# Kernel optimization log

Measured on AMD Instinct MI355X. Metric: run time of the kernel, lower is better.

Reference implementation:

```python
import jax, jax.numpy as jnp
import numpy as np

B, L, D, H, HD = 2, 2048, 768, 12, 64
NEG = -1e9

def _rotate_half(x):
    x1, x2 = jnp.split(x, 2, axis=-1)
    return jnp.concatenate([-x2, x1], axis=-1)

def setup_inputs() -> dict:
    key = jax.random.key(0)
    ks = jax.random.split(key, 8)
    hidden_states = jax.random.normal(ks[0], (B, L, D), dtype=jnp.float32)
    # additive causal mask [B,1,L,L]
    causal = jnp.where(jnp.tril(jnp.ones((L, L), dtype=bool)), 0.0, NEG).astype(jnp.float32)
    attention_mask = jnp.broadcast_to(causal[None, None], (B, 1, L, L))
    # RoPE tables [B, L, HD]
    inv_freq = 1.0 / (10000.0 ** (jnp.arange(0, HD, 2, dtype=jnp.float32) / HD))
    angles = jnp.arange(L, dtype=jnp.float32)[:, None] * inv_freq[None, :]  # [L, HD/2]
    emb = jnp.concatenate([angles, angles], axis=-1)  # [L, HD]
    cos = jnp.broadcast_to(jnp.cos(emb)[None], (B, L, HD))
    sin = jnp.broadcast_to(jnp.sin(emb)[None], (B, L, HD))
    s = 0.02
    Wq = s * jax.random.normal(ks[1], (H * HD, D), dtype=jnp.float32)
    Wk = s * jax.random.normal(ks[2], (H * HD, D), dtype=jnp.float32)
    Wv = s * jax.random.normal(ks[3], (H * HD, D), dtype=jnp.float32)
    Wo = s * jax.random.normal(ks[4], (D, H * HD), dtype=jnp.float32)
    return {"hidden_states": hidden_states, "attention_mask": attention_mask,
            "cos": cos, "sin": sin, "Wq": Wq, "Wk": Wk, "Wv": Wv, "Wo": Wo}

def reference(hidden_states, attention_mask, cos, sin, Wq, Wk, Wv, Wo):
    b, l, _ = hidden_states.shape
    def proj(W):  # silu(x @ W.T) -> [B, H, L, HD]
        y = jax.nn.silu(jnp.einsum('bld,ed->ble', hidden_states, W))
        return y.reshape(b, l, H, HD).transpose(0, 2, 1, 3)
    q, k, v = proj(Wq), proj(Wk), proj(Wv)
    c = cos[:, None]  # [B,1,L,HD]
    s = sin[:, None]
    q = q * c + _rotate_half(q) * s
    k = k * c + _rotate_half(k) * s
    attn = jnp.einsum('bhqd,bhkd->bhqk', q, k)
    attn = attn + attention_mask
    attn = jax.nn.silu(attn) / l
    out = jnp.einsum('bhqk,bhkd->bhqd', attn, v)  # [B,H,L,HD]
    out = out.transpose(0, 2, 1, 3).reshape(b, l, H * HD)
    attn_output = jnp.einsum('ble,de->bld', out, Wo)
    return attn_output, attn
```

## Files before the change

kernel.cpp:

```cpp
#include <hip/hip_runtime.h>
#include <cstddef>

#define Bc   2
#define Lc   2048
#define Dc   768
#define Hc   12
#define HDc  64
#define Mrows (Bc * Lc)
#define PAD  72

typedef _Float16 half8 __attribute__((ext_vector_type(8)));
typedef unsigned short ushort8 __attribute__((ext_vector_type(8)));
typedef __attribute__((ext_vector_type(4))) float floatx4;

__device__ __forceinline__ float silu_f(float x) {
    return x / (1.0f + __expf(-x));
}
__device__ __forceinline__ unsigned short f2h(float x) {
    _Float16 h = (_Float16)x;
    return __builtin_bit_cast(unsigned short, h);
}
__device__ __forceinline__ float h2f(unsigned short u) {
    return (float)__builtin_bit_cast(_Float16, u);
}

template<int MODE>
__global__ __launch_bounds__(256)
void gemm_f16(const float* __restrict__ A32, const unsigned short* __restrict__ A16,
              const float* __restrict__ W, void* __restrict__ Cout) {
    __shared__ unsigned short Af[64][PAD];
    __shared__ unsigned short Wf[64][PAD];
    const int tid  = threadIdx.x;
    const int lane = tid & 63, w = tid >> 6;
    const int m    = lane & 15, quad = lane >> 4;
    const int m0 = blockIdx.y * 64, n0 = blockIdx.x * 64;

    floatx4 acc[4] = {{0.f,0.f,0.f,0.f},{0.f,0.f,0.f,0.f},
                      {0.f,0.f,0.f,0.f},{0.f,0.f,0.f,0.f}};

    for (int kc = 0; kc < Dc; kc += 64) {
        __syncthreads();
        if (MODE == 2) {
#pragma unroll
            for (int p = 0; p < 2; ++p) {
                const int f = tid + p * 256;
                const int row = f >> 3, c8 = (f & 7) << 3;
                const ushort8 t = *(const ushort8*)(A16 + (size_t)(m0 + row) * Dc + kc + c8);
                *(ushort8*)&Af[row][c8] = t;
            }
        } else {
#pragma unroll
            for (int p = 0; p < 4; ++p) {
                const int f = tid + p * 256;
                const int row = f >> 4, c4 = (f & 15) << 2;
                const float4 t = *(const float4*)(A32 + (size_t)(m0 + row) * Dc + kc + c4);
                const ushort4 hh = make_ushort4(f2h(t.x), f2h(t.y), f2h(t.z), f2h(t.w));
                *(ushort4*)&Af[row][c4] = hh;
            }
        }
#pragma unroll
        for (int p = 0; p < 4; ++p) {
            const int f = tid + p * 256;
            const int row = f >> 4, c4 = (f & 15) << 2;
            const float4 t = *(const float4*)(W + (size_t)(n0 + row) * Dc + kc + c4);
            const ushort4 hh = make_ushort4(f2h(t.x), f2h(t.y), f2h(t.z), f2h(t.w));
            *(ushort4*)&Wf[row][c4] = hh;
        }
        __syncthreads();

        const half8 a0 = *(const half8*)&Af[w * 16 + m][0 * 32 + quad * 8];
        const half8 a1 = *(const half8*)&Af[w * 16 + m][1 * 32 + quad * 8];
#pragma unroll
        for (int nn = 0; nn < 4; ++nn) {
            const half8 b0 = *(const half8*)&Wf[nn * 16 + m][0 * 32 + quad * 8];
            const half8 b1 = *(const half8*)&Wf[nn * 16 + m][1 * 32 + quad * 8];
            acc[nn] = __builtin_amdgcn_mfma_f32_16x16x32_f16(a0, b0, acc[nn], 0, 0, 0);
            acc[nn] = __builtin_amdgcn_mfma_f32_16x16x32_f16(a1, b1, acc[nn], 0, 0, 0);
        }
    }

#pragma unroll
    for (int nn = 0; nn < 4; ++nn) {
        const int col = n0 + nn * 16 + m;
        if (MODE == 0) {
            const int h = col >> 6, hd = col & 63;
            unsigned short* q16 = (unsigned short*)Cout;
#pragma unroll
            for (int r = 0; r < 4; ++r) {
                const int row = m0 + w * 16 + quad * 4 + r;
                const int b = row >> 11, l = row & (Lc - 1);
                q16[(((size_t)(b * Hc + h) * Lc + l) * HDc) + hd] = f2h(silu_f(acc[nn][r]));
            }
        } else if (MODE == 1) {
            const int h = col >> 6, hd = col & 63;
            unsigned short* vT16 = (unsigned short*)Cout;
            const int row0 = m0 + w * 16 + quad * 4;
            const int b = row0 >> 11, l0 = row0 & (Lc - 1);
            const ushort4 hh = make_ushort4(f2h(silu_f(acc[nn][0])), f2h(silu_f(acc[nn][1])),
                                            f2h(silu_f(acc[nn][2])), f2h(silu_f(acc[nn][3])));
            *(ushort4*)(vT16 + ((size_t)(b * Hc + h) * HDc + hd) * Lc + l0) = hh;
        } else {
            float* C = (float*)Cout;
#pragma unroll
            for (int r = 0; r < 4; ++r) {
                const int row = m0 + w * 16 + quad * 4 + r;
                C[(size_t)row * Dc + col] = acc[nn][r];
            }
        }
    }
}

__global__ __launch_bounds__(256)
void rope_kernel(unsigned short* __restrict__ q, unsigned short* __restrict__ k,
                 const float* __restrict__ cosb, const float* __restrict__ sinb) {
    const int idx = blockIdx.x * blockDim.x + threadIdx.x;
    const int total = Bc * Hc * Lc * 32;
    if (idx >= total) return;
    const int hd = idx & 31;
    const int l  = (idx >> 5) & (Lc - 1);
    const int h  = (idx >> 16) % Hc;
    const int b  = idx / (32 * Lc * Hc);
    unsigned short* arr = (blockIdx.y == 0) ? q : k;
    const size_t base  = (((size_t)b * Hc + h) * Lc + l) * HDc;
    const size_t cbase = ((size_t)b * Lc + l) * HDc;
    const float x1 = h2f(arr[base + hd]);
    const float x2 = h2f(arr[base + hd + 32]);
    const float c1 = cosb[cbase + hd],      s1 = sinb[cbase + hd];
    const float c2 = cosb[cbase + hd + 32], s2 = sinb[cbase + hd + 32];
    arr[base + hd]      = f2h(x1 * c1 - x2 * s1);
    arr[base + hd + 32] = f2h(x2 * c2 + x1 * s2);
}

__global__ __launch_bounds__(256)
void attn_kernel(const unsigned short* __restrict__ q16,
                 const unsigned short* __restrict__ k16,
                 const unsigned short* __restrict__ vT16,
                 float* __restrict__ attn_out,
                 unsigned short* __restrict__ o16) {
    __shared__ unsigned short Qf[64][PAD];
    __shared__ unsigned short Kf[64][PAD];
    __shared__ unsigned short Vt[64][PAD];
    __shared__ unsigned short Ps[64][PAD];

    const int tid  = threadIdx.x;
    const int lane = tid & 63, w = tid >> 6;
    const int m = lane & 15, quad = lane >> 4;
    const int qt = gridDim.x - 1 - blockIdx.x;
    const int bh = blockIdx.y;
    const int b = bh / Hc, h = bh % Hc;
    const size_t qkv = (size_t)bh * Lc * HDc;
    const float invL = 1.0f / (float)Lc;

    {
        const unsigned short* qp = q16 + qkv + (size_t)(qt * 64) * HDc;
#pragma unroll
        for (int p = 0; p < 2; ++p) {
            const int f = tid + p * 256;
            const int row = f >> 3, c8 = (f & 7) << 3;
            *(ushort8*)&Qf[row][c8] = *(const ushort8*)(qp + row * HDc + c8);
        }
    }
    __syncthreads();

    const half8 bq0 = *(const half8*)&Qf[w * 16 + m][0 * 32 + quad * 8];
    const half8 bq1 = *(const half8*)&Qf[w * 16 + m][1 * 32 + quad * 8];

    floatx4 oacc[4] = {{0.f,0.f,0.f,0.f},{0.f,0.f,0.f,0.f},
                       {0.f,0.f,0.f,0.f},{0.f,0.f,0.f,0.f}};
    float* attn_base = attn_out + (size_t)bh * Lc * Lc;

    for (int kt = 0; kt <= qt; ++kt) {
        __syncthreads();
        {
            const unsigned short* kp = k16 + qkv + (size_t)(kt * 64) * HDc;
            const unsigned short* vp = vT16 + (size_t)bh * HDc * Lc + kt * 64;
#pragma unroll
            for (int p = 0; p < 2; ++p) {
                const int f = tid + p * 256;
                const int row = f >> 3, c8 = (f & 7) << 3;
                *(ushort8*)&Kf[row][c8] = *(const ushort8*)(kp + row * HDc + c8);
                *(ushort8*)&Vt[row][c8] = *(const ushort8*)(vp + (size_t)row * Lc + c8);
            }
        }
        __syncthreads();

        const bool diag = (kt == qt);
        const int gi = qt * 64 + w * 16 + m;
#pragma unroll
        for (int mm = 0; mm < 4; ++mm) {
            const half8 ak0 = *(const half8*)&Kf[mm * 16 + m][0 * 32 + quad * 8];
            const half8 ak1 = *(const half8*)&Kf[mm * 16 + m][1 * 32 + quad * 8];
            floatx4 s = {0.f, 0.f, 0.f, 0.f};
            s = __builtin_amdgcn_mfma_f32_16x16x32_f16(ak0, bq0, s, 0, 0, 0);
            s = __builtin_amdgcn_mfma_f32_16x16x32_f16(ak1, bq1, s, 0, 0, 0);
            const int kj0 = mm * 16 + quad * 4;
            const int gj0 = kt * 64 + kj0;
            float v[4];
#pragma unroll
            for (int r = 0; r < 4; ++r) {
                float val = s[r];
                v[r] = (diag && (gj0 + r) > gi) ? 0.0f : silu_f(val) * invL;
            }
            *(float4*)(attn_base + (size_t)gi * Lc + gj0) = make_float4(v[0], v[1], v[2], v[3]);
            *(ushort4*)&Ps[w * 16 + m][kj0] = make_ushort4(f2h(v[0]), f2h(v[1]), f2h(v[2]), f2h(v[3]));
        }
        __syncthreads();

        const half8 ap0 = *(const half8*)&Ps[w * 16 + m][0 * 32 + quad * 8];
        const half8 ap1 = *(const half8*)&Ps[w * 16 + m][1 * 32 + quad * 8];
#pragma unroll
        for (int nn = 0; nn < 4; ++nn) {
            const half8 bv0 = *(const half8*)&Vt[nn * 16 + m][0 * 32 + quad * 8];
            const half8 bv1 = *(const half8*)&Vt[nn * 16 + m][1 * 32 + quad * 8];
            oacc[nn] = __builtin_amdgcn_mfma_f32_16x16x32_f16(ap0, bv0, oacc[nn], 0, 0, 0);
            oacc[nn] = __builtin_amdgcn_mfma_f32_16x16x32_f16(ap1, bv1, oacc[nn], 0, 0, 0);
        }
    }

    {
        const int tx = tid & 15, ty = tid >> 4;
#pragma unroll 1
        for (int kt2 = qt + 1; kt2 < Lc / 64; ++kt2) {
            const float4 z = make_float4(0.f, 0.f, 0.f, 0.f);
#pragma unroll
            for (int i = 0; i < 4; ++i) {
                const int gi2 = qt * 64 + (ty << 2) + i;
                *(float4*)(attn_base + (size_t)gi2 * Lc + kt2 * 64 + (tx << 2)) = z;
            }
        }
    }

#pragma unroll
    for (int nn = 0; nn < 4; ++nn)
#pragma unroll
        for (int r = 0; r < 4; ++r) {
            const int gi2 = qt * 64 + w * 16 + quad * 4 + r;
            o16[((size_t)b * Lc + gi2) * Dc + h * HDc + nn * 16 + m] = f2h(oacc[nn][r]);
        }
}

extern "C" void kernel_launch(void* const* d_in, const int* in_sizes, int n_in,
                              void* d_out, int out_size, void* d_ws, size_t ws_size,
                              hipStream_t stream) {
    const float* hs   = (const float*)d_in[0];
    const float* cosb = (const float*)d_in[2];
    const float* sinb = (const float*)d_in[3];
    const float* Wq   = (const float*)d_in[4];
    const float* Wk   = (const float*)d_in[5];
    const float* Wv   = (const float*)d_in[6];
    const float* Wo   = (const float*)d_in[7];

    float* attn_output = (float*)d_out;
    float* attn        = attn_output + (size_t)Mrows * Dc;

    const size_t seg = (size_t)Bc * Hc * Lc * HDc;
    unsigned short* q16  = (unsigned short*)d_ws;
    unsigned short* k16  = q16 + seg;
    unsigned short* vT16 = k16 + seg;
    unsigned short* o16  = vT16 + seg;

    const dim3 blk(256);
    const dim3 ggrid(Dc / 64, Mrows / 64);

    gemm_f16<0><<<ggrid, blk, 0, stream>>>(hs, nullptr, Wq, q16);
    gemm_f16<0><<<ggrid, blk, 0, stream>>>(hs, nullptr, Wk, k16);
    gemm_f16<1><<<ggrid, blk, 0, stream>>>(hs, nullptr, Wv, vT16);

    const int total = Bc * Hc * Lc * 32;
    rope_kernel<<<dim3((total + 255) / 256, 2), blk, 0, stream>>>(q16, k16, cosb, sinb);

    attn_kernel<<<dim3(Lc / 64, Bc * Hc), blk, 0, stream>>>(q16, k16, vT16, attn, o16);

    gemm_f16<2><<<ggrid, blk, 0, stream>>>(nullptr, o16, Wo, attn_output);
}
```

Baseline: 690.3 us.

## Fuse QKV projections with RoPE, prefetch K/V in attention, use nontemporal stores

The three Q/K/V projection GEMMs are merged into one launch, and RoPE is applied in the epilogue, so the separate rope kernel and its extra read/write pass over q and k go away. The attention kernel now prefetches the next K/V tile into registers while the current tile is being computed, and it drops the barrier between writing P and reading it, since each wave reads back only the rows it wrote. The large attention-matrix writes and the output GEMM stores use nontemporal stores to reduce cache pollution. Together these aim to cut launch count, memory traffic and synchronisation stalls, at the cost of more register pressure.

```diff
diff --git a/kernel.cpp b/kernel.cpp
--- a/kernel.cpp
+++ b/kernel.cpp
@@ -20,115 +20,82 @@
     _Float16 h = (_Float16)x;
     return __builtin_bit_cast(unsigned short, h);
 }
-__device__ __forceinline__ float h2f(unsigned short u) {
-    return (float)__builtin_bit_cast(_Float16, u);
-}
-
-template<int MODE>
+
 __global__ __launch_bounds__(256)
-void gemm_f16(const float* __restrict__ A32, const unsigned short* __restrict__ A16,
-              const float* __restrict__ W, void* __restrict__ Cout) {
+void gemm_qkv(const float* __restrict__ hs,
+              const float* __restrict__ Wq, const float* __restrict__ Wk,
+              const float* __restrict__ Wv,
+              const float* __restrict__ cosb, const float* __restrict__ sinb,
+              unsigned short* __restrict__ q16, unsigned short* __restrict__ k16,
+              unsigned short* __restrict__ vT16) {
     __shared__ unsigned short Af[64][PAD];
     __shared__ unsigned short Wf[64][PAD];
     const int tid  = threadIdx.x;
     const int lane = tid & 63, w = tid >> 6;
-    const int m    = lane & 15, quad = lane >> 4;
-    const int m0 = blockIdx.y * 64, n0 = blockIdx.x * 64;
+    const int m = lane & 15, quad = lane >> 4;
+    const int m0 = blockIdx.y * 64;
+    const int nblk = blockIdx.x;
+    const int which = nblk / 12;
+    const int n0 = (nblk - which * 12) * 64;
+    const float* __restrict__ W = (which == 0) ? Wq : (which == 1) ? Wk : Wv;
 
     floatx4 acc[4] = {{0.f,0.f,0.f,0.f},{0.f,0.f,0.f,0.f},
                       {0.f,0.f,0.f,0.f},{0.f,0.f,0.f,0.f}};
 
     for (int kc = 0; kc < Dc; kc += 64) {
         __syncthreads();
-        if (MODE == 2) {
-#pragma unroll
-            for (int p = 0; p < 2; ++p) {
-                const int f = tid + p * 256;
-                const int row = f >> 3, c8 = (f & 7) << 3;
-                const ushort8 t = *(const ushort8*)(A16 + (size_t)(m0 + row) * Dc + kc + c8);
-                *(ushort8*)&Af[row][c8] = t;
-            }
-        } else {
-#pragma unroll
-            for (int p = 0; p < 4; ++p) {
-                const int f = tid + p * 256;
-                const int row = f >> 4, c4 = (f & 15) << 2;
-                const float4 t = *(const float4*)(A32 + (size_t)(m0 + row) * Dc + kc + c4);
-                const ushort4 hh = make_ushort4(f2h(t.x), f2h(t.y), f2h(t.z), f2h(t.w));
-                *(ushort4*)&Af[row][c4] = hh;
-            }
-        }
 #pragma unroll
         for (int p = 0; p < 4; ++p) {
             const int f = tid + p * 256;
             const int row = f >> 4, c4 = (f & 15) << 2;
-            const float4 t = *(const float4*)(W + (size_t)(n0 + row) * Dc + kc + c4);
-            const ushort4 hh = make_ushort4(f2h(t.x), f2h(t.y), f2h(t.z), f2h(t.w));
-            *(ushort4*)&Wf[row][c4] = hh;
-        }
-        __syncthreads();
-
-        const half8 a0 = *(const half8*)&Af[w * 16 + m][0 * 32 + quad * 8];
-        const half8 a1 = *(const half8*)&Af[w * 16 + m][1 * 32 + quad * 8];
+            const float4 ta = *(const float4*)(hs + (size_t)(m0 + row) * Dc + kc + c4);
+            *(ushort4*)&Af[row][c4] = make_ushort4(f2h(ta.x), f2h(ta.y), f2h(ta.z), f2h(ta.w));
+            const float4 tw = *(const float4*)(W + (size_t)(n0 + row) * Dc + kc + c4);
+            *(ushort4*)&Wf[row][c4] = make_ushort4(f2h(tw.x), f2h(tw.y), f2h(tw.z), f2h(tw.w));
+        }
+        __syncthreads();
+
+        const half8 a0 = *(const half8*)&Af[w * 16 + m][quad * 8];
+        const half8 a1 = *(const half8*)&Af[w * 16 + m][32 + quad * 8];
 #pragma unroll
         for (int nn = 0; nn < 4; ++nn) {
-            const half8 b0 = *(const half8*)&Wf[nn * 16 + m][0 * 32 + quad * 8];
-            const half8 b1 = *(const half8*)&Wf[nn * 16 + m][1 * 32 + quad * 8];
+            const half8 b0 = *(const half8*)&Wf[nn * 16 + m][quad * 8];
+            const half8 b1 = *(const half8*)&Wf[nn * 16 + m][32 + quad * 8];
             acc[nn] = __builtin_amdgcn_mfma_f32_16x16x32_f16(a0, b0, acc[nn], 0, 0, 0);
             acc[nn] = __builtin_amdgcn_mfma_f32_16x16x32_f16(a1, b1, acc[nn], 0, 0, 0);
         }
     }
 
-#pragma unroll
-    for (int nn = 0; nn < 4; ++nn) {
-        const int col = n0 + nn * 16 + m;
-        if (MODE == 0) {
+    if (which < 2) {
+        unsigned short* __restrict__ dst = which ? k16 : q16;
+        const int h = n0 >> 6;
+#pragma unroll
+        for (int r = 0; r < 4; ++r) {
+            const int row = m0 + w * 16 + quad * 4 + r;
+            const int b = row >> 11, l = row & (Lc - 1);
+            const size_t cb   = ((size_t)b * Lc + l) * HDc;
+            const size_t base = ((size_t)(b * Hc + h) * Lc + l) * HDc;
+            const float ya = silu_f(acc[0][r]);
+            const float yb = silu_f(acc[1][r]);
+            const float yc = silu_f(acc[2][r]);
+            const float yd = silu_f(acc[3][r]);
+            dst[base + m]      = f2h(ya * cosb[cb + m]      - yc * sinb[cb + m]);
+            dst[base + m + 16] = f2h(yb * cosb[cb + m + 16] - yd * sinb[cb + m + 16]);
+            dst[base + m + 32] = f2h(yc * cosb[cb + m + 32] + ya * sinb[cb + m + 32]);
+            dst[base + m + 48] = f2h(yd * cosb[cb + m + 48] + yb * sinb[cb + m + 48]);
+        }
+    } else {
+#pragma unroll
+        for (int nn = 0; nn < 4; ++nn) {
+            const int col = n0 + nn * 16 + m;
             const int h = col >> 6, hd = col & 63;
-            unsigned short* q16 = (unsigned short*)Cout;
-#pragma unroll
-            for (int r = 0; r < 4; ++r) {
-                const int row = m0 + w * 16 + quad * 4 + r;
-                const int b = row >> 11, l = row & (Lc - 1);
-                q16[(((size_t)(b * Hc + h) * Lc + l) * HDc) + hd] = f2h(silu_f(acc[nn][r]));
-            }
-        } else if (MODE == 1) {
-            const int h = col >> 6, hd = col & 63;
-            unsigned short* vT16 = (unsigned short*)Cout;
             const int row0 = m0 + w * 16 + quad * 4;
             const int b = row0 >> 11, l0 = row0 & (Lc - 1);
             const ushort4 hh = make_ushort4(f2h(silu_f(acc[nn][0])), f2h(silu_f(acc[nn][1])),
                                             f2h(silu_f(acc[nn][2])), f2h(silu_f(acc[nn][3])));
             *(ushort4*)(vT16 + ((size_t)(b * Hc + h) * HDc + hd) * Lc + l0) = hh;
-        } else {
-            float* C = (float*)Cout;
-#pragma unroll
-            for (int r = 0; r < 4; ++r) {
-                const int row = m0 + w * 16 + quad * 4 + r;
-                C[(size_t)row * Dc + col] = acc[nn][r];
-            }
-        }
-    }
-}
-
-__global__ __launch_bounds__(256)
-void rope_kernel(unsigned short* __restrict__ q, unsigned short* __restrict__ k,
-                 const float* __restrict__ cosb, const float* __restrict__ sinb) {
-    const int idx = blockIdx.x * blockDim.x + threadIdx.x;
-    const int total = Bc * Hc * Lc * 32;
-    if (idx >= total) return;
-    const int hd = idx & 31;
-    const int l  = (idx >> 5) & (Lc - 1);
-    const int h  = (idx >> 16) % Hc;
-    const int b  = idx / (32 * Lc * Hc);
-    unsigned short* arr = (blockIdx.y == 0) ? q : k;
-    const size_t base  = (((size_t)b * Hc + h) * Lc + l) * HDc;
-    const size_t cbase = ((size_t)b * Lc + l) * HDc;
-    const float x1 = h2f(arr[base + hd]);
-    const float x2 = h2f(arr[base + hd + 32]);
-    const float c1 = cosb[cbase + hd],      s1 = sinb[cbase + hd];
-    const float c2 = cosb[cbase + hd + 32], s2 = sinb[cbase + hd + 32];
-    arr[base + hd]      = f2h(x1 * c1 - x2 * s1);
-    arr[base + hd + 32] = f2h(x2 * c2 + x1 * s2);
+        }
+    }
 }
 
 __global__ __launch_bounds__(256)
@@ -147,49 +114,54 @@
     const int m = lane & 15, quad = lane >> 4;
     const int qt = gridDim.x - 1 - blockIdx.x;
     const int bh = blockIdx.y;
-    const int b = bh / Hc, h = bh % Hc;
+    const int b = bh / Hc, h = bh - b * Hc;
     const size_t qkv = (size_t)bh * Lc * HDc;
     const float invL = 1.0f / (float)Lc;
 
+    const int srow = tid >> 3, sc8 = (tid & 7) << 3;
+    const unsigned short* kbase = k16 + qkv;
+    const unsigned short* vbase = vT16 + (size_t)bh * HDc * Lc;
+
     {
         const unsigned short* qp = q16 + qkv + (size_t)(qt * 64) * HDc;
-#pragma unroll
-        for (int p = 0; p < 2; ++p) {
-            const int f = tid + p * 256;
-            const int row = f >> 3, c8 = (f & 7) << 3;
-            *(ushort8*)&Qf[row][c8] = *(const ushort8*)(qp + row * HDc + c8);
-        }
-    }
+        *(ushort8*)&Qf[srow][sc8]      = *(const ushort8*)(qp + srow * HDc + sc8);
+        *(ushort8*)&Qf[srow + 32][sc8] = *(const ushort8*)(qp + (srow + 32) * HDc + sc8);
+    }
+
+    ushort8 kreg0, kreg1, vreg0, vreg1;
+    kreg0 = *(const ushort8*)(kbase + srow * HDc + sc8);
+    kreg1 = *(const ushort8*)(kbase + (srow + 32) * HDc + sc8);
+    vreg0 = *(const ushort8*)(vbase + (size_t)srow * Lc + sc8);
+    vreg1 = *(const ushort8*)(vbase + (size_t)(srow + 32) * Lc + sc8);
+    *(ushort8*)&Kf[srow][sc8]      = kreg0;
+    *(ushort8*)&Kf[srow + 32][sc8] = kreg1;
+    *(ushort8*)&Vt[srow][sc8]      = vreg0;
+    *(ushort8*)&Vt[srow + 32][sc8] = vreg1;
     __syncthreads();
 
-    const half8 bq0 = *(const half8*)&Qf[w * 16 + m][0 * 32 + quad * 8];
-    const half8 bq1 = *(const half8*)&Qf[w * 16 + m][1 * 32 + quad * 8];
+    const half8 bq0 = *(const half8*)&Qf[w * 16 + m][quad * 8];
+    const half8 bq1 = *(const half8*)&Qf[w * 16 + m][32 + quad * 8];
 
     floatx4 oacc[4] = {{0.f,0.f,0.f,0.f},{0.f,0.f,0.f,0.f},
                        {0.f,0.f,0.f,0.f},{0.f,0.f,0.f,0.f}};
     float* attn_base = attn_out + (size_t)bh * Lc * Lc;
+    const int gi = qt * 64 + w * 16 + m;
 
     for (int kt = 0; kt <= qt; ++kt) {
-        __syncthreads();
-        {
-            const unsigned short* kp = k16 + qkv + (size_t)(kt * 64) * HDc;
-            const unsigned short* vp = vT16 + (size_t)bh * HDc * Lc + kt * 64;
-#pragma unroll
-            for (int p = 0; p < 2; ++p) {
-                const int f = tid + p * 256;
-                const int row = f >> 3, c8 = (f & 7) << 3;
-                *(ushort8*)&Kf[row][c8] = *(const ushort8*)(kp + row * HDc + c8);
-                *(ushort8*)&Vt[row][c8] = *(const ushort8*)(vp + (size_t)row * Lc + c8);
-            }
-        }
-        __syncthreads();
+        if (kt < qt) {
+            const unsigned short* kp = kbase + (size_t)((kt + 1) * 64) * HDc;
+            const unsigned short* vp = vbase + (kt + 1) * 64;
+            kreg0 = *(const ushort8*)(kp + srow * HDc + sc8);
+            kreg1 = *(const ushort8*)(kp + (srow + 32) * HDc + sc8);
+            vreg0 = *(const ushort8*)(vp + (size_t)srow * Lc + sc8);
+            vreg1 = *(const ushort8*)(vp + (size_t)(srow + 32) * Lc + sc8);
+        }
 
         const bool diag = (kt == qt);
-        const int gi = qt * 64 + w * 16 + m;
 #pragma unroll
         for (int mm = 0; mm < 4; ++mm) {
-            const half8 ak0 = *(const half8*)&Kf[mm * 16 + m][0 * 32 + quad * 8];
-            const half8 ak1 = *(const half8*)&Kf[mm * 16 + m][1 * 32 + quad * 8];
+            const half8 ak0 = *(const half8*)&Kf[mm * 16 + m][quad * 8];
+            const half8 ak1 = *(const half8*)&Kf[mm * 16 + m][32 + quad * 8];
             floatx4 s = {0.f, 0.f, 0.f, 0.f};
             s = __builtin_amdgcn_mfma_f32_16x16x32_f16(ak0, bq0, s, 0, 0, 0);
             s = __builtin_amdgcn_mfma_f32_16x16x32_f16(ak1, bq1, s, 0, 0, 0);
@@ -201,31 +173,41 @@
                 float val = s[r];
                 v[r] = (diag && (gj0 + r) > gi) ? 0.0f : silu_f(val) * invL;
             }
-            *(float4*)(attn_base + (size_t)gi * Lc + gj0) = make_float4(v[0], v[1], v[2], v[3]);
+            const floatx4 vv = {v[0], v[1], v[2], v[3]};
+            __builtin_nontemporal_store(vv, (floatx4*)(attn_base + (size_t)gi * Lc + gj0));
             *(ushort4*)&Ps[w * 16 + m][kj0] = make_ushort4(f2h(v[0]), f2h(v[1]), f2h(v[2]), f2h(v[3]));
         }
-        __syncthreads();
-
-        const half8 ap0 = *(const half8*)&Ps[w * 16 + m][0 * 32 + quad * 8];
-        const half8 ap1 = *(const half8*)&Ps[w * 16 + m][1 * 32 + quad * 8];
+
+        const half8 ap0 = *(const half8*)&Ps[w * 16 + m][quad * 8];
+        const half8 ap1 = *(const half8*)&Ps[w * 16 + m][32 + quad * 8];
 #pragma unroll
         for (int nn = 0; nn < 4; ++nn) {
-            const half8 bv0 = *(const half8*)&Vt[nn * 16 + m][0 * 32 + quad * 8];
-            const half8 bv1 = *(const half8*)&Vt[nn * 16 + m][1 * 32 + quad * 8];
+            const half8 bv0 = *(const half8*)&Vt[nn * 16 + m][quad * 8];
+            const half8 bv1 = *(const half8*)&Vt[nn * 16 + m][32 + quad * 8];
             oacc[nn] = __builtin_amdgcn_mfma_f32_16x16x32_f16(ap0, bv0, oacc[nn], 0, 0, 0);
             oacc[nn] = __builtin_amdgcn_mfma_f32_16x16x32_f16(ap1, bv1, oacc[nn], 0, 0, 0);
         }
+
+        __syncthreads();
+        if (kt < qt) {
+            *(ushort8*)&Kf[srow][sc8]      = kreg0;
+            *(ushort8*)&Kf[srow + 32][sc8] = kreg1;
+            *(ushort8*)&Vt[srow][sc8]      = vreg0;
+            *(ushort8*)&Vt[srow + 32][sc8] = vreg1;
+            __syncthreads();
+        }
     }
 
     {
         const int tx = tid & 15, ty = tid >> 4;
+        const floatx4 z = {0.f, 0.f, 0.f, 0.f};
 #pragma unroll 1
         for (int kt2 = qt + 1; kt2 < Lc / 64; ++kt2) {
-            const float4 z = make_float4(0.f, 0.f, 0.f, 0.f);
 #pragma unroll
             for (int i = 0; i < 4; ++i) {
                 const int gi2 = qt * 64 + (ty << 2) + i;
-                *(float4*)(attn_base + (size_t)gi2 * Lc + kt2 * 64 + (tx << 2)) = z;
+                __builtin_nontemporal_store(z,
+                    (floatx4*)(attn_base + (size_t)gi2 * Lc + kt2 * 64 + (tx << 2)));
             }
         }
     }
@@ -237,6 +219,58 @@
             const int gi2 = qt * 64 + w * 16 + quad * 4 + r;
             o16[((size_t)b * Lc + gi2) * Dc + h * HDc + nn * 16 + m] = f2h(oacc[nn][r]);
         }
+}
+
+__global__ __launch_bounds__(256)
+void gemm_out(const unsigned short* __restrict__ A16, const float* __restrict__ W,
+              float* __restrict__ C) {
+    __shared__ unsigned short Af[64][PAD];
+    __shared__ unsigned short Wf[64][PAD];
+    const int tid  = threadIdx.x;
+    const int lane = tid & 63, w = tid >> 6;
+    const int m = lane & 15, quad = lane >> 4;
+    const int m0 = blockIdx.y * 64, n0 = blockIdx.x * 64;
+
+    floatx4 acc[4] = {{0.f,0.f,0.f,0.f},{0.f,0.f,0.f,0.f},
+                      {0.f,0.f,0.f,0.f},{0.f,0.f,0.f,0.f}};
+
+    for (int kc = 0; kc < Dc; kc += 64) {
+        __syncthreads();
+#pragma unroll
+        for (int p = 0; p < 2; ++p) {
+            const int f = tid + p * 256;
+            const int row = f >> 3, c8 = (f & 7) << 3;
+            *(ushort8*)&Af[row][c8] = *(const ushort8*)(A16 + (size_t)(m0 + row) * Dc + kc + c8);
+        }
+#pragma unroll
+        for (int p = 0; p < 4; ++p) {
+            const int f = tid + p * 256;
+            const int row = f >> 4, c4 = (f & 15) << 2;
+            const float4 t = *(const float4*)(W + (size_t)(n0 + row) * Dc + kc + c4);
+            *(ushort4*)&Wf[row][c4] = make_ushort4(f2h(t.x), f2h(t.y), f2h(t.z), f2h(t.w));
+        }
+        __syncthreads();
+
+        const half8 a0 = *(const half8*)&Af[w * 16 + m][quad * 8];
+        const half8 a1 = *(const half8*)&Af[w * 16 + m][32 + quad * 8];
+#pragma unroll
+        for (int nn = 0; nn < 4; ++nn) {
+            const half8 b0 = *(const half8*)&Wf[nn * 16 + m][quad * 8];
+            const half8 b1 = *(const half8*)&Wf[nn * 16 + m][32 + quad * 8];
+            acc[nn] = __builtin_amdgcn_mfma_f32_16x16x32_f16(a0, b0, acc[nn], 0, 0, 0);
+            acc[nn] = __builtin_amdgcn_mfma_f32_16x16x32_f16(a1, b1, acc[nn], 0, 0, 0);
+        }
+    }
+
+#pragma unroll
+    for (int nn = 0; nn < 4; ++nn) {
+        const int col = n0 + nn * 16 + m;
+#pragma unroll
+        for (int r = 0; r < 4; ++r) {
+            const int row = m0 + w * 16 + quad * 4 + r;
+            __builtin_nontemporal_store(acc[nn][r], C + (size_t)row * Dc + col);
+        }
+    }
 }
 
 extern "C" void kernel_launch(void* const* d_in, const int* in_sizes, int n_in,
@@ -260,16 +294,9 @@
     unsigned short* o16  = vT16 + seg;
 
     const dim3 blk(256);
-    const dim3 ggrid(Dc / 64, Mrows / 64);
-
-    gemm_f16<0><<<ggrid, blk, 0, stream>>>(hs, nullptr, Wq, q16);
-    gemm_f16<0><<<ggrid, blk, 0, stream>>>(hs, nullptr, Wk, k16);
-    gemm_f16<1><<<ggrid, blk, 0, stream>>>(hs, nullptr, Wv, vT16);
-
-    const int total = Bc * Hc * Lc * 32;
-    rope_kernel<<<dim3((total + 255) / 256, 2), blk, 0, stream>>>(q16, k16, cosb, sinb);
-
+
+    gemm_qkv<<<dim3(36, Mrows / 64), blk, 0, stream>>>(hs, Wq, Wk, Wv, cosb, sinb,
+                                                       q16, k16, vT16);
     attn_kernel<<<dim3(Lc / 64, Bc * Hc), blk, 0, stream>>>(q16, k16, vT16, attn, o16);
-
-    gemm_f16<2><<<ggrid, blk, 0, stream>>>(nullptr, o16, Wo, attn_output);
-}
+    gemm_out<<<dim3(Dc / 64, Mrows / 64), blk, 0, stream>>>(o16, Wo, attn_output);
+}
```

Result: faster. 593.1 us (-14.1%).
